# Kernel tuning notes

Hardware: AMD Instinct MI355X
Metric: run time of the kernel (lower is better)

## Reference

```python
import jax, jax.numpy as jnp
import numpy as np

D = 512; NH = 8; FF = 2048; LE = 6; LD = 6; V = 97; SM = 512; SQ = 128; B = 16
EPS = 1e-5


def _posenc(length, depth):
    half = depth // 2
    pos = jnp.arange(length, dtype=jnp.float32)[:, None]
    dep = jnp.arange(half, dtype=jnp.float32)[None, :] / half
    ang = pos / (10000.0 ** dep)
    return jnp.concatenate([jnp.sin(ang), jnp.cos(ang)], axis=-1)  # [length, depth]


def _ln(x, w, b):
    mu = jnp.mean(x, axis=-1, keepdims=True)
    var = jnp.mean((x - mu) ** 2, axis=-1, keepdims=True)
    return (x - mu) * jax.lax.rsqrt(var + EPS) * w + b


def _heads(t, S, Bt):
    return t.reshape(S, Bt * NH, D // NH).transpose(1, 0, 2)  # [B*H, S, dk]


def _self_attn(x, wqkv, bqkv, wo, bo, causal):
    S, Bt, _ = x.shape
    qkv = x @ wqkv.T + bqkv
    q, k, v = jnp.split(qkv, 3, axis=-1)
    q = _heads(q, S, Bt); k = _heads(k, S, Bt); v = _heads(v, S, Bt)
    scores = jnp.einsum('hqd,hkd->hqk', q, k) / jnp.sqrt(jnp.asarray(D // NH, x.dtype))
    if causal:
        mask = jnp.triu(jnp.ones((S, S), bool), 1)
        scores = jnp.where(mask[None], -jnp.inf, scores)
    attn = jax.nn.softmax(scores, axis=-1)
    out = jnp.einsum('hqk,hkd->hqd', attn, v).transpose(1, 0, 2).reshape(S, Bt, D)
    return out @ wo.T + bo


def _cross_attn(query, memory, wq, bq, wk, bk, wv, bv, wo, bo):
    Sq, Bt, _ = query.shape
    Sm = memory.shape[0]
    q = _heads(query @ wq.T + bq, Sq, Bt)
    k = _heads(memory @ wk.T + bk, Sm, Bt)
    v = _heads(memory @ wv.T + bv, Sm, Bt)
    scores = jnp.einsum('hqd,hkd->hqk', q, k) / jnp.sqrt(jnp.asarray(D // NH, query.dtype))
    attn = jax.nn.softmax(scores, axis=-1)
    out = jnp.einsum('hqk,hkd->hqd', attn, v).transpose(1, 0, 2).reshape(Sq, Bt, D)
    return out @ wo.T + bo


def _forward(src, tokens, tok_emb,
             enc_qkv_w, enc_qkv_b, enc_out_w, enc_out_b,
             enc_l1_w, enc_l1_b, enc_l2_w, enc_l2_b,
             enc_n1_w, enc_n1_b, enc_n2_w, enc_n2_b,
             dec_qkv_w, dec_qkv_b, dec_sout_w, dec_sout_b,
             dec_q_w, dec_q_b, dec_k_w, dec_k_b, dec_v_w, dec_v_b,
             dec_cout_w, dec_cout_b,
             dec_l1_w, dec_l1_b, dec_l2_w, dec_l2_b,
             dec_n1_w, dec_n1_b, dec_n2_w, dec_n2_b, dec_n3_w, dec_n3_b,
             out_w, out_b):
    # ---- encoder ----
    x = src  # [SM, B, D]
    for i in range(LE):
        x2 = _self_attn(x, enc_qkv_w[i], enc_qkv_b[i], enc_out_w[i], enc_out_b[i], causal=False)
        x = _ln(x + x2, enc_n1_w[i], enc_n1_b[i])
        x2 = jax.nn.relu(x @ enc_l1_w[i].T + enc_l1_b[i]) @ enc_l2_w[i].T + enc_l2_b[i]
        x = _ln(x + x2, enc_n2_w[i], enc_n2_b[i])
    memory = x
    # ---- decoder ----
    tgt = tok_emb[tokens] + _posenc(tokens.shape[0], D)[:, None, :]  # [SQ, B, D]
    for i in range(LD):
        x2 = _self_attn(tgt, dec_qkv_w[i], dec_qkv_b[i], dec_sout_w[i], dec_sout_b[i], causal=True)
        tgt = _ln(tgt + x2, dec_n1_w[i], dec_n1_b[i])
        x2 = _cross_attn(tgt, memory, dec_q_w[i], dec_q_b[i], dec_k_w[i], dec_k_b[i],
                         dec_v_w[i], dec_v_b[i], dec_cout_w[i], dec_cout_b[i])
        tgt = _ln(tgt + x2, dec_n2_w[i], dec_n2_b[i])
        x2 = jax.nn.relu(tgt @ dec_l1_w[i].T + dec_l1_b[i]) @ dec_l2_w[i].T + dec_l2_b[i]
        tgt = _ln(tgt + x2, dec_n3_w[i], dec_n3_b[i])
    return tgt @ out_w.T + out_b  # [SQ, B, V]


def setup_inputs() -> dict:
    key = jax.random.key(0)
    ks = iter(jax.random.split(key, 64))
    g = lambda shape: jax.random.normal(next(ks), shape, dtype=jnp.float32) * 0.02
    inp = {
        'src': jax.random.normal(next(ks), (SM, B, D), dtype=jnp.float32),
        'tokens': jax.random.randint(next(ks), (SQ, B), 0, V),
        'tok_emb': g((V, D)),
        'enc_qkv_w': g((LE, 3 * D, D)), 'enc_qkv_b': g((LE, 3 * D)),
        'enc_out_w': g((LE, D, D)), 'enc_out_b': g((LE, D)),
        'enc_l1_w': g((LE, FF, D)), 'enc_l1_b': g((LE, FF)),
        'enc_l2_w': g((LE, D, FF)), 'enc_l2_b': g((LE, D)),
        'enc_n1_w': jnp.ones((LE, D)), 'enc_n1_b': jnp.zeros((LE, D)),
        'enc_n2_w': jnp.ones((LE, D)), 'enc_n2_b': jnp.zeros((LE, D)),
        'dec_qkv_w': g((LD, 3 * D, D)), 'dec_qkv_b': g((LD, 3 * D)),
        'dec_sout_w': g((LD, D, D)), 'dec_sout_b': g((LD, D)),
        'dec_q_w': g((LD, D, D)), 'dec_q_b': g((LD, D)),
        'dec_k_w': g((LD, D, D)), 'dec_k_b': g((LD, D)),
        'dec_v_w': g((LD, D, D)), 'dec_v_b': g((LD, D)),
        'dec_cout_w': g((LD, D, D)), 'dec_cout_b': g((LD, D)),
        'dec_l1_w': g((LD, FF, D)), 'dec_l1_b': g((LD, FF)),
        'dec_l2_w': g((LD, D, FF)), 'dec_l2_b': g((LD, D)),
        'dec_n1_w': jnp.ones((LD, D)), 'dec_n1_b': jnp.zeros((LD, D)),
        'dec_n2_w': jnp.ones((LD, D)), 'dec_n2_b': jnp.zeros((LD, D)),
        'dec_n3_w': jnp.ones((LD, D)), 'dec_n3_b': jnp.zeros((LD, D)),
        'out_w': g((V, D)), 'out_b': g((V,)),
    }
    return inp


def reference(src, tokens, tok_emb,
              enc_qkv_w, enc_qkv_b, enc_out_w, enc_out_b,
              enc_l1_w, enc_l1_b, enc_l2_w, enc_l2_b,
              enc_n1_w, enc_n1_b, enc_n2_w, enc_n2_b,
              dec_qkv_w, dec_qkv_b, dec_sout_w, dec_sout_b,
              dec_q_w, dec_q_b, dec_k_w, dec_k_b, dec_v_w, dec_v_b,
              dec_cout_w, dec_cout_b,
              dec_l1_w, dec_l1_b, dec_l2_w, dec_l2_b,
              dec_n1_w, dec_n1_b, dec_n2_w, dec_n2_b, dec_n3_w, dec_n3_b,
              out_w, out_b):
    return _forward(src, tokens, tok_emb,
                    enc_qkv_w, enc_qkv_b, enc_out_w, enc_out_b,
                    enc_l1_w, enc_l1_b, enc_l2_w, enc_l2_b,
                    enc_n1_w, enc_n1_b, enc_n2_w, enc_n2_b,
                    dec_qkv_w, dec_qkv_b, dec_sout_w, dec_sout_b,
                    dec_q_w, dec_q_b, dec_k_w, dec_k_b, dec_v_w, dec_v_b,
                    dec_cout_w, dec_cout_b,
                    dec_l1_w, dec_l1_b, dec_l2_w, dec_l2_b,
                    dec_n1_w, dec_n1_b, dec_n2_w, dec_n2_b, dec_n3_w, dec_n3_b,
                    out_w, out_b)
```

## Files before the change

kernel.cpp:

```cpp
#include <hip/hip_runtime.h>
#include <hip/hip_bf16.h>
#include <cstddef>
#include <cstdint>

#define D_MODEL 512
#define BATCH 16
#define EPS_LN 1e-5f

typedef __bf16 bf16x8 __attribute__((ext_vector_type(8)));
typedef float f32x4 __attribute__((ext_vector_type(4)));
typedef unsigned short u16x8 __attribute__((ext_vector_type(8)));
typedef unsigned short u16x4 __attribute__((ext_vector_type(4)));
typedef unsigned short u16x2 __attribute__((ext_vector_type(2)));

__device__ __forceinline__ void gload_lds16(const void* g, void* l) {
    __builtin_amdgcn_global_load_lds(
        (const __attribute__((address_space(1))) void*)g,
        (__attribute__((address_space(3))) void*)l,
        16, 0, 0);
}

template <int BM, int OUTBF16, int SWAP>
__global__ __launch_bounds__(512) void gemm_mfma(
    const __bf16* __restrict__ A, const __bf16* __restrict__ W,
    const __bf16* __restrict__ W2, int wsplit,
    const float* __restrict__ bias, const float* __restrict__ bias2, int bsplit,
    void* __restrict__ Cout, __bf16* __restrict__ VTout, int m_vt0, int log2S,
    int N, int Mlim, int MS, int K, int relu, int permrow)
{
    constexpr int MR     = BM / 32;
    constexpr int WRSPAN = BM / 2;
    constexpr int ABYTES = BM * 128;
    constexpr int PA     = ABYTES / 8192;
    constexpr int BUFB   = ABYTES + 16384;

    __shared__ __align__(16) char smem[2 * BUFB];

    const int tid  = threadIdx.x;
    const int lane = tid & 63;
    const int wid  = tid >> 6;
    const int wrow = wid >> 2;
    const int wcol = wid & 3;
    const int row0 = blockIdx.y * BM;
    const int col0 = blockIdx.x * 128;

    const int lrow  = lane & 15;
    const int lhalf = lane >> 4;
    const int koff0 = ((lhalf) ^ (lrow & 7)) * 16;
    const int koff1 = ((4 + lhalf) ^ (lrow & 7)) * 16;

    const int srow = tid >> 3;
    const int slot = tid & 7;
    const int sg   = slot ^ (srow & 7);

    f32x4 acc[MR][2] = {};

    const __bf16* Wsel = W;
    int wc0 = col0;
    if (col0 >= wsplit) { Wsel = W2; wc0 = col0 - wsplit; }

    const __bf16* Abase = A + (size_t)(row0 + srow) * K + sg * 8;
    const __bf16* Wbase = Wsel + (size_t)(wc0 + srow) * K + sg * 8;

    auto stage = [&](char* buf, int kt) {
#pragma unroll
        for (int p = 0; p < PA; ++p)
            gload_lds16(Abase + (size_t)p * 64 * K + kt, buf + p * 8192 + tid * 16);
#pragma unroll
        for (int p = 0; p < 2; ++p)
            gload_lds16(Wbase + (size_t)p * 64 * K + kt,
                        buf + ABYTES + p * 8192 + tid * 16);
    };

    stage(smem, 0);
    const int nkt = K >> 6;
    int cur = 0;
    for (int kt = 0; kt < nkt; ++kt) {
        __syncthreads();
        if (kt + 1 < nkt) stage(smem + (cur ^ 1) * BUFB, (kt + 1) * 64);
        const char* aB = smem + cur * BUFB + (wrow * WRSPAN + lrow) * 128;
        const char* wB = smem + cur * BUFB + ABYTES + (wcol * 32 + lrow) * 128;
#pragma unroll
        for (int ks = 0; ks < 2; ++ks) {
            const int ko = ks ? koff1 : koff0;
            bf16x8 af[MR], bfr[2];
#pragma unroll
            for (int m = 0; m < MR; ++m) af[m]  = *(const bf16x8*)(aB + m * 2048 + ko);
#pragma unroll
            for (int n = 0; n < 2; ++n)  bfr[n] = *(const bf16x8*)(wB + n * 2048 + ko);
            if (SWAP) {
#pragma unroll
                for (int m = 0; m < MR; ++m)
#pragma unroll
                    for (int n = 0; n < 2; ++n)
                        acc[m][n] = __builtin_amdgcn_mfma_f32_16x16x32_bf16(
                            bfr[n], af[m], acc[m][n], 0, 0, 0);
            } else {
#pragma unroll
                for (int m = 0; m < MR; ++m)
#pragma unroll
                    for (int n = 0; n < 2; ++n)
                        acc[m][n] = __builtin_amdgcn_mfma_f32_16x16x32_bf16(
                            af[m], bfr[n], acc[m][n], 0, 0, 0);
            }
        }
        cur ^= 1;
    }

    if (SWAP) {
#pragma unroll
        for (int m = 0; m < MR; ++m) {
            const int r = row0 + wrow * WRSPAN + m * 16 + lrow;
#pragma unroll
            for (int n = 0; n < 2; ++n) {
                const int c0 = col0 + wcol * 32 + n * 16 + lhalf * 4;
                const float4 bv = *(const float4*)(bias + c0);
                float o0 = acc[m][n][0] + bv.x, o1 = acc[m][n][1] + bv.y;
                float o2 = acc[m][n][2] + bv.z, o3 = acc[m][n][3] + bv.w;
                if (relu) {
                    o0 = fmaxf(o0, 0.f); o1 = fmaxf(o1, 0.f);
                    o2 = fmaxf(o2, 0.f); o3 = fmaxf(o3, 0.f);
                }
                if (OUTBF16) {
                    union { __bf16 h4[4]; u16x4 u; } pk;
                    pk.h4[0] = (__bf16)o0; pk.h4[1] = (__bf16)o1;
                    pk.h4[2] = (__bf16)o2; pk.h4[3] = (__bf16)o3;
                    *(u16x4*)((__bf16*)Cout + (size_t)r * MS + c0) = pk.u;
                } else {
                    *(float4*)((float*)Cout + (size_t)r * MS + c0) =
                        make_float4(o0, o1, o2, o3);
                }
            }
        }
    } else {
        const int orow = row0 + wrow * WRSPAN + lhalf * 4;
        const int ocol = col0 + wcol * 32 + lrow;
        const int smask = (1 << log2S) - 1;
#pragma unroll
        for (int n = 0; n < 2; ++n) {
            const int c = ocol + n * 16;
            if (c >= m_vt0) {
                const int cv = c - m_vt0;
                const int hh = cv >> 6, dd = cv & 63;
                const float bv = (bias2 && c >= bsplit) ? bias2[c - bsplit] : bias[c];
#pragma unroll
                for (int m = 0; m < MR; ++m) {
                    const int rr = orow + m * 16;
                    const int bb = rr >> log2S, ss = rr & smask;
                    union { __bf16 h4[4]; u16x4 u; } pk;
#pragma unroll
                    for (int j = 0; j < 4; ++j)
                        pk.h4[j] = (__bf16)(acc[m][n][j] + bv);
                    *(u16x4*)(VTout + (((size_t)((bb * 8 + hh) * 64 + dd)) << log2S) + ss) = pk.u;
                }
            } else if (c < Mlim) {
                const float bv = (bias2 && c >= bsplit) ? bias2[c - bsplit] : bias[c];
#pragma unroll
                for (int m = 0; m < MR; ++m) {
#pragma unroll
                    for (int j = 0; j < 4; ++j) {
                        int rr = orow + m * 16 + j;
                        if (permrow) rr = ((rr & smask) * BATCH) + (rr >> log2S);
                        float v = acc[m][n][j] + bv;
                        if (relu) v = fmaxf(v, 0.f);
                        if (OUTBF16) ((__bf16*)Cout)[(size_t)rr * MS + c] = (__bf16)v;
                        else         ((float*)Cout)[(size_t)rr * MS + c] = v;
                    }
                }
            }
        }
    }
}

template <int CAUSAL>
__global__ __launch_bounds__(256) void attn_mfma(
    const __bf16* __restrict__ Qb, const __bf16* __restrict__ Kb,
    const __bf16* __restrict__ VT, __bf16* __restrict__ Op,
    int Sq, int Skv, int qstride, int kstride, int koff, float scale)
{
    __shared__ __align__(16) char smem[40960];
    const int tid = threadIdx.x;
    const int l   = tid & 63;
    const int w   = tid >> 6;
    char* Psm = smem + 32768 + w * 2048;

    const int qc = blockIdx.x;
    const int h  = blockIdx.y;
    const int b  = blockIdx.z;
    const int l15 = l & 15;
    const int g   = l >> 4;
    const int sw  = l15 & 7;

    const int sq = qc * 64 + w * 16 + l15;
    const __bf16* qrow = Qb + ((size_t)(b * Sq + sq)) * qstride + h * 64 + g * 8;
    const bf16x8 qf0 = *(const bf16x8*)(qrow);
    const bf16x8 qf1 = *(const bf16x8*)(qrow + 32);

    const int srow = tid >> 3;
    const int slot = tid & 7;

    auto stageKV = [&](char* buf, int kc) {
#pragma unroll
        for (int p = 0; p < 2; ++p) {
            const int r   = p * 32 + srow;
            const int sgo = (slot ^ (r & 7)) * 8;
            const __bf16* ksrc = Kb + ((size_t)(b * Skv + kc * 64 + r)) * kstride
                                    + koff + h * 64 + sgo;
            gload_lds16(ksrc, buf + (p * 256 + tid) * 16);
            const __bf16* vsrc = VT + ((size_t)((b * 8 + h) * 64 + r)) * Skv
                                    + kc * 64 + sgo;
            gload_lds16(vsrc, buf + 8192 + (p * 256 + tid) * 16);
        }
    };

    f32x4 acc[4] = {};
    float m_run = -1e30f, l_run = 0.f;

    const int nkc = CAUSAL ? (qc + 1) : (Skv >> 6);
    stageKV(smem, 0);
    int cur = 0;
    for (int kc = 0; kc < nkc; ++kc) {
        __syncthreads();
        if (kc + 1 < nkc) stageKV(smem + (cur ^ 1) * 16384, kc + 1);
        const char* Ksm = smem + cur * 16384;
        const char* Vsm = Ksm + 8192;

        f32x4 st[4];
#pragma unroll
        for (int f = 0; f < 4; ++f) {
            const char* kr = Ksm + (f * 16 + l15) * 128;
            bf16x8 ka0 = *(const bf16x8*)(kr + ((g ^ sw) * 16));
            bf16x8 ka1 = *(const bf16x8*)(kr + (((4 + g) ^ sw) * 16));
            f32x4 z = {};
            z = __builtin_amdgcn_mfma_f32_16x16x32_bf16(ka0, qf0, z, 0, 0, 0);
            st[f] = __builtin_amdgcn_mfma_f32_16x16x32_bf16(ka1, qf1, z, 0, 0, 0);
        }

        float rmax = -1e30f;
#pragma unroll
        for (int f = 0; f < 4; ++f)
#pragma unroll
            for (int j = 0; j < 4; ++j) {
                float v = st[f][j] * scale;
                if (CAUSAL) {
                    if (kc * 64 + f * 16 + g * 4 + j > sq) v = -1e30f;
                }
                st[f][j] = v;
                rmax = fmaxf(rmax, v);
            }
        rmax = fmaxf(rmax, __shfl_xor(rmax, 16, 64));
        rmax = fmaxf(rmax, __shfl_xor(rmax, 32, 64));
        const float mn = fmaxf(m_run, rmax);
        const float corr = __expf(m_run - mn);
        m_run = mn;
        float rsum = 0.f;
#pragma unroll
        for (int f = 0; f < 4; ++f)
#pragma unroll
            for (int j = 0; j < 4; ++j) {
                float p = __expf(st[f][j] - mn);
                st[f][j] = p;
                rsum += p;
            }
        rsum += __shfl_xor(rsum, 16, 64);
        rsum += __shfl_xor(rsum, 32, 64);
        l_run = l_run * corr + rsum;

#pragma unroll
        for (int j = 0; j < 4; ++j) {
            const float cj = __shfl(corr, g * 20 + j, 64);
            acc[0][j] *= cj; acc[1][j] *= cj; acc[2][j] *= cj; acc[3][j] *= cj;
        }

#pragma unroll
        for (int f = 0; f < 4; ++f)
#pragma unroll
            for (int j2 = 0; j2 < 2; ++j2) {
                union { __bf16 h2[2]; unsigned u; } cv;
                cv.h2[0] = (__bf16)st[f][2 * j2];
                cv.h2[1] = (__bf16)st[f][2 * j2 + 1];
                const int key0 = 16 * f + 4 * g + 2 * j2;
                const int byte = l15 * 128 + (((key0 >> 3) ^ sw) * 16) + (key0 & 7) * 2;
                *(unsigned*)(Psm + byte) = cv.u;
            }

#pragma unroll
        for (int ks = 0; ks < 2; ++ks) {
            const int so = ((4 * ks + g) ^ sw) * 16;
            bf16x8 pa = *(const bf16x8*)(Psm + l15 * 128 + so);
#pragma unroll
            for (int n = 0; n < 4; ++n) {
                bf16x8 vb = *(const bf16x8*)(Vsm + (n * 16 + l15) * 128 + so);
                acc[n] = __builtin_amdgcn_mfma_f32_16x16x32_bf16(pa, vb, acc[n], 0, 0, 0);
            }
        }
        cur ^= 1;
    }

    const float inv = 1.f / l_run;
#pragma unroll
    for (int j = 0; j < 4; ++j) {
        const float ij = __shfl(inv, g * 20 + j, 64);
        const int s = qc * 64 + w * 16 + g * 4 + j;
        __bf16* orow = Op + ((size_t)(b * Sq + s)) * D_MODEL + h * 64 + l15;
#pragma unroll
        for (int n = 0; n < 4; ++n)
            orow[n * 16] = (__bf16)(acc[n][j] * ij);
    }
}

__global__ __launch_bounds__(256) void add_ln(
    const float* __restrict__ X, const __bf16* __restrict__ Y,
    const float* __restrict__ w, const float* __restrict__ bias,
    float* __restrict__ Of, __bf16* __restrict__ Oh)
{
    const int t   = blockIdx.x;
    const int tid = threadIdx.x;
    const float2 x2 = *(const float2*)(X + (size_t)t * D_MODEL + tid * 2);
    const u16x2 yv = *(const u16x2*)(Y + (size_t)t * D_MODEL + tid * 2);
    union { u16x2 u; __bf16 h2[2]; } yc; yc.u = yv;
    float v0 = x2.x + (float)yc.h2[0], v1 = x2.y + (float)yc.h2[1];
    float sum = v0 + v1;
    float sq  = v0 * v0 + v1 * v1;
#pragma unroll
    for (int off = 32; off; off >>= 1) {
        sum += __shfl_xor(sum, off);
        sq  += __shfl_xor(sq, off);
    }
    __shared__ float ssum[4], ssq[4];
    const int wid = tid >> 6;
    if ((tid & 63) == 0) { ssum[wid] = sum; ssq[wid] = sq; }
    __syncthreads();
    sum = ssum[0] + ssum[1] + ssum[2] + ssum[3];
    sq  = ssq[0] + ssq[1] + ssq[2] + ssq[3];

    const float mu  = sum * (1.f / D_MODEL);
    const float var = sq * (1.f / D_MODEL) - mu * mu;
    const float rs  = rsqrtf(var + EPS_LN);
    const float2 w2 = *(const float2*)(w + tid * 2);
    const float2 b2 = *(const float2*)(bias + tid * 2);
    float o0 = (v0 - mu) * rs * w2.x + b2.x;
    float o1 = (v1 - mu) * rs * w2.y + b2.y;
    *(float2*)(Of + (size_t)t * D_MODEL + tid * 2) = make_float2(o0, o1);
    union { __bf16 h2[2]; u16x2 u; } cv;
    cv.h2[0] = (__bf16)o0; cv.h2[1] = (__bf16)o1;
    *(u16x2*)(Oh + (size_t)t * D_MODEL + tid * 2) = cv.u;
}

__global__ __launch_bounds__(256) void permute_src(
    const float* __restrict__ src, float* __restrict__ Of, __bf16* __restrict__ Oh)
{
    const int t = blockIdx.x;
    const int b = t >> 9, s = t & 511;
    const int tid = threadIdx.x;
    const float2 v = *(const float2*)(src + ((size_t)(s * BATCH + b)) * D_MODEL + tid * 2);
    *(float2*)(Of + (size_t)t * D_MODEL + tid * 2) = v;
    union { __bf16 h2[2]; u16x2 u; } cv;
    cv.h2[0] = (__bf16)v.x; cv.h2[1] = (__bf16)v.y;
    *(u16x2*)(Oh + (size_t)t * D_MODEL + tid * 2) = cv.u;
}

__global__ __launch_bounds__(256) void embed_pos(
    const int* __restrict__ tokens, const float* __restrict__ emb,
    float* __restrict__ Of, __bf16* __restrict__ Oh)
{
    const int t   = blockIdx.x;
    const int b   = t >> 7, s = t & 127;
    const int tid = threadIdx.x;
    const int tok = tokens[s * BATCH + b];
    const float C = 9.210340371976184f / 256.f;
    const int d = tid * 2;
    const int j = (d < 256) ? d : (d - 256);
    float a0 = (float)s * expf(-(float)j * C);
    float a1 = (float)s * expf(-(float)(j + 1) * C);
    float pe0 = (d < 256) ? sinf(a0) : cosf(a0);
    float pe1 = (d < 256) ? sinf(a1) : cosf(a1);
    const float2 e2 = *(const float2*)(emb + (size_t)tok * D_MODEL + d);
    float o0 = e2.x + pe0, o1 = e2.y + pe1;
    *(float2*)(Of + (size_t)t * D_MODEL + d) = make_float2(o0, o1);
    union { __bf16 h2[2]; u16x2 u; } cv;
    cv.h2[0] = (__bf16)o0; cv.h2[1] = (__bf16)o1;
    *(u16x2*)(Oh + (size_t)t * D_MODEL + d) = cv.u;
}

struct CvtSeg { const float* s; __bf16* d; int n8; };
struct CvtArgs { CvtSeg seg[12]; int tot8; };

__global__ __launch_bounds__(256) void cvt_multi(CvtArgs a)
{
    const int stride = gridDim.x * 256;
    int sgi = 0;
    int base = 0;
    for (int u = blockIdx.x * 256 + threadIdx.x; u < a.tot8; u += stride) {
        while (u - base >= a.seg[sgi].n8) { base += a.seg[sgi].n8; ++sgi; }
        const int v = u - base;
        const float4 f0 = ((const float4*)a.seg[sgi].s)[v * 2];
        const float4 f1 = ((const float4*)a.seg[sgi].s)[v * 2 + 1];
        union { __bf16 h[8]; u16x8 u; } c;
        c.h[0] = (__bf16)f0.x; c.h[1] = (__bf16)f0.y;
        c.h[2] = (__bf16)f0.z; c.h[3] = (__bf16)f0.w;
        c.h[4] = (__bf16)f1.x; c.h[5] = (__bf16)f1.y;
        c.h[6] = (__bf16)f1.z; c.h[7] = (__bf16)f1.w;
        ((u16x8*)a.seg[sgi].d)[v] = c.u;
    }
}

__global__ __launch_bounds__(256) void pad_outw(
    const float* __restrict__ w, __bf16* __restrict__ o)
{
    const int idx = blockIdx.x * 256 + threadIdx.x;
    const int r = idx >> 9;
    const int c = idx & 511;
    o[idx] = (__bf16)(r < 97 ? w[r * 512 + c] : 0.f);
}

extern "C" void kernel_launch(void* const* d_in, const int* in_sizes, int n_in,
                              void* d_out, int out_size, void* d_ws, size_t ws_size,
                              hipStream_t stream)
{
    const float* src     = (const float*)d_in[0];
    const int*   tokens  = (const int*)d_in[1];
    const float* tok_emb = (const float*)d_in[2];
    const float* enc_qkv_w = (const float*)d_in[3];
    const float* enc_qkv_b = (const float*)d_in[4];
    const float* enc_out_w = (const float*)d_in[5];
    const float* enc_out_b = (const float*)d_in[6];
    const float* enc_l1_w  = (const float*)d_in[7];
    const float* enc_l1_b  = (const float*)d_in[8];
    const float* enc_l2_w  = (const float*)d_in[9];
    const float* enc_l2_b  = (const float*)d_in[10];
    const float* enc_n1_w  = (const float*)d_in[11];
    const float* enc_n1_b  = (const float*)d_in[12];
    const float* enc_n2_w  = (const float*)d_in[13];
    const float* enc_n2_b  = (const float*)d_in[14];
    const float* dec_qkv_w = (const float*)d_in[15];
    const float* dec_qkv_b = (const float*)d_in[16];
    const float* dec_sout_w = (const float*)d_in[17];
    const float* dec_sout_b = (const float*)d_in[18];
    const float* dec_q_w   = (const float*)d_in[19];
    const float* dec_q_b   = (const float*)d_in[20];
    const float* dec_k_w   = (const float*)d_in[21];
    const float* dec_k_b   = (const float*)d_in[22];
    const float* dec_v_w   = (const float*)d_in[23];
    const float* dec_v_b   = (const float*)d_in[24];
    const float* dec_cout_w = (const float*)d_in[25];
    const float* dec_cout_b = (const float*)d_in[26];
    const float* dec_l1_w  = (const float*)d_in[27];
    const float* dec_l1_b  = (const float*)d_in[28];
    const float* dec_l2_w  = (const float*)d_in[29];
    const float* dec_l2_b  = (const float*)d_in[30];
    const float* dec_n1_w  = (const float*)d_in[31];
    const float* dec_n1_b  = (const float*)d_in[32];
    const float* dec_n2_w  = (const float*)d_in[33];
    const float* dec_n2_b  = (const float*)d_in[34];
    const float* dec_n3_w  = (const float*)d_in[35];
    const float* dec_n3_b  = (const float*)d_in[36];
    const float* out_w     = (const float*)d_in[37];
    const float* out_b     = (const float*)d_in[38];

    const int NE = 512 * BATCH;
    const int ND = 128 * BATCH;
    const float scale = 0.125f;
    const int BIG = 1 << 30;

    char* w8 = (char*)d_ws;
    float*  Ax_f = (float*) (w8 + 0);
    float*  T_f  = (float*) (w8 + 16777216);
    __bf16* Ax_h = (__bf16*)(w8 + 20971520);
    __bf16* T_h  = (__bf16*)(w8 + 29360128);
    __bf16* AO_h = (__bf16*)(w8 + 31457280);
    __bf16* Y_h  = (__bf16*)(w8 + 39845888);
    __bf16* VT   = (__bf16*)(w8 + 48234496);
    __bf16* OWp  = (__bf16*)(w8 + 56623104);
    char*   Gb   = w8 + 56754176;
    __bf16* Gqk  = (__bf16*)Gb;
    __bf16* Gh   = (__bf16*)Gb;
    __bf16* Gq   = (__bf16*)Gb;
    __bf16* Gk   = (__bf16*)(Gb + 2097152);
    __bf16* WB   = (__bf16*)(w8 + 90308608);

    const bool upfront = ws_size >= (size_t)178388992;

    auto gemmS = [&](const __bf16* Am, const __bf16* Wm, const float* bv,
                     void* C, int N, int M, int K, int relu) {
        const int nb128 = (M / 128) * (N / 128);
        if (nb128 >= 512) {
            dim3 grid(M / 128, N / 128);
            gemm_mfma<128, 1, 1><<<grid, 512, 0, stream>>>(
                Am, Wm, nullptr, BIG, bv, nullptr, 0, C, nullptr, BIG, 0,
                N, M, M, K, relu, 0);
        } else {
            dim3 grid(M / 128, N / 64);
            gemm_mfma<64, 1, 1><<<grid, 512, 0, stream>>>(
                Am, Wm, nullptr, BIG, bv, nullptr, 0, C, nullptr, BIG, 0,
                N, M, M, K, relu, 0);
        }
    };
    auto gemmN = [&](const __bf16* Am, const __bf16* Wm, const __bf16* W2m, int wsplit,
                     const float* bv, const float* bv2, int bsplit,
                     void* C, __bf16* VTp, int m_vt0, int log2S,
                     int N, int M, int MS, int K, bool outbf, int permrow) {
        const int nb128 = ((M + 127) / 128) * (N / 128);
        if (nb128 >= 512) {
            dim3 grid((M + 127) / 128, N / 128);
            if (outbf) gemm_mfma<128, 1, 0><<<grid, 512, 0, stream>>>(
                Am, Wm, W2m, wsplit, bv, bv2, bsplit, C, VTp, m_vt0, log2S,
                N, M, MS, K, 0, permrow);
            else       gemm_mfma<128, 0, 0><<<grid, 512, 0, stream>>>(
                Am, Wm, W2m, wsplit, bv, bv2, bsplit, C, VTp, m_vt0, log2S,
                N, M, MS, K, 0, permrow);
        } else {
            dim3 grid((M + 127) / 128, N / 64);
            if (outbf) gemm_mfma<64, 1, 0><<<grid, 512, 0, stream>>>(
                Am, Wm, W2m, wsplit, bv, bv2, bsplit, C, VTp, m_vt0, log2S,
                N, M, MS, K, 0, permrow);
            else       gemm_mfma<64, 0, 0><<<grid, 512, 0, stream>>>(
                Am, Wm, W2m, wsplit, bv, bv2, bsplit, C, VTp, m_vt0, log2S,
                N, M, MS, K, 0, permrow);
        }
    };
    auto cvt = [&](CvtArgs& a, int blocks) {
        int tot = 0;
        for (int i = 0; i < 12; ++i) tot += a.seg[i].n8;
        a.tot8 = tot;
        cvt_multi<<<blocks, 256, 0, stream>>>(a);
    };

    permute_src<<<NE, 256, 0, stream>>>(src, Ax_f, Ax_h);
    pad_outw<<<256, 256, 0, stream>>>(out_w, OWp);

    __bf16* WencQKV = WB;
    __bf16* WencOUT = WencQKV + 4718592;
    __bf16* WencL1  = WencOUT + 1572864;
    __bf16* WencL2  = WencL1 + 6291456;
    __bf16* WdecQKV = WencL2 + 6291456;
    __bf16* WdecSOUT = WdecQKV + 4718592;
    __bf16* WdecQ   = WdecSOUT + 1572864;
    __bf16* WdecK   = WdecQ + 1572864;
    __bf16* WdecV   = WdecK + 1572864;
    __bf16* WdecCOUT = WdecV + 1572864;
    __bf16* WdecL1  = WdecCOUT + 1572864;
    __bf16* WdecL2  = WdecL1 + 6291456;

    if (upfront) {
        CvtArgs a = {};
        a.seg[0]  = { enc_qkv_w,  WencQKV,  4718592 / 8 };
        a.seg[1]  = { enc_out_w,  WencOUT,  1572864 / 8 };
        a.seg[2]  = { enc_l1_w,   WencL1,   6291456 / 8 };
        a.seg[3]  = { enc_l2_w,   WencL2,   6291456 / 8 };
        a.seg[4]  = { dec_qkv_w,  WdecQKV,  4718592 / 8 };
        a.seg[5]  = { dec_sout_w, WdecSOUT, 1572864 / 8 };
        a.seg[6]  = { dec_q_w,    WdecQ,    1572864 / 8 };
        a.seg[7]  = { dec_k_w,    WdecK,    1572864 / 8 };
        a.seg[8]  = { dec_v_w,    WdecV,    1572864 / 8 };
        a.seg[9]  = { dec_cout_w, WdecCOUT, 1572864 / 8 };
        a.seg[10] = { dec_l1_w,   WdecL1,   6291456 / 8 };
        a.seg[11] = { dec_l2_w,   WdecL2,   6291456 / 8 };
        cvt(a, 4096);
    }

    for (int i = 0; i < 6; ++i) {
        __bf16 *wqkv, *wout, *wl1, *wl2;
        if (upfront) {
            wqkv = WencQKV + (size_t)i * 786432;
            wout = WencOUT + (size_t)i * 262144;
            wl1  = WencL1 + (size_t)i * 1048576;
            wl2  = WencL2 + (size_t)i * 1048576;
        } else {
            wqkv = WB; wout = WB + 786432; wl1 = WB + 1048576; wl2 = WB + 2097152;
            CvtArgs a = {};
            a.seg[0] = { enc_qkv_w + (size_t)i * 786432,  wqkv, 786432 / 8 };
            a.seg[1] = { enc_out_w + (size_t)i * 262144,  wout, 262144 / 8 };
            a.seg[2] = { enc_l1_w  + (size_t)i * 1048576, wl1, 1048576 / 8 };
            a.seg[3] = { enc_l2_w  + (size_t)i * 1048576, wl2, 1048576 / 8 };
            cvt(a, 1024);
        }

        gemmN(Ax_h, wqkv, nullptr, BIG, enc_qkv_b + (size_t)i * 1536, nullptr, 0,
              Gqk, VT, 1024, 9, NE, 1536, 1024, 512, true, 0);
        attn_mfma<0><<<dim3(8, 8, BATCH), 256, 0, stream>>>(
            Gqk, Gqk, VT, AO_h, 512, 512, 1024, 1024, 512, scale);
        gemmS(AO_h, wout, enc_out_b + (size_t)i * 512, Y_h, NE, 512, 512, 0);
        add_ln<<<NE, 256, 0, stream>>>(Ax_f, Y_h,
                                       enc_n1_w + (size_t)i * 512, enc_n1_b + (size_t)i * 512,
                                       Ax_f, Ax_h);
        gemmS(Ax_h, wl1, enc_l1_b + (size_t)i * 2048, Gh, NE, 2048, 512, 1);
        gemmS(Gh, wl2, enc_l2_b + (size_t)i * 512, Y_h, NE, 512, 2048, 0);
        add_ln<<<NE, 256, 0, stream>>>(Ax_f, Y_h,
                                       enc_n2_w + (size_t)i * 512, enc_n2_b + (size_t)i * 512,
                                       Ax_f, Ax_h);
    }

    embed_pos<<<ND, 256, 0, stream>>>(tokens, tok_emb, T_f, T_h);
    for (int i = 0; i < 6; ++i) {
        __bf16 *dqkv, *dsout, *dq, *dk, *dv, *dcout, *dl1, *dl2;
        if (upfront) {
            dqkv  = WdecQKV + (size_t)i * 786432;
            dsout = WdecSOUT + (size_t)i * 262144;
            dq    = WdecQ + (size_t)i * 262144;
            dk    = WdecK + (size_t)i * 262144;
            dv    = WdecV + (size_t)i * 262144;
            dcout = WdecCOUT + (size_t)i * 262144;
            dl1   = WdecL1 + (size_t)i * 1048576;
            dl2   = WdecL2 + (size_t)i * 1048576;
        } else {
            dqkv = WB; dsout = WB + 786432; dq = WB + 1048576; dk = WB + 1310720;
            dv = WB + 1572864; dcout = WB + 1835008; dl1 = WB + 2097152; dl2 = WB + 3145728;
            CvtArgs a = {};
            a.seg[0] = { dec_qkv_w  + (size_t)i * 786432,  dqkv,  786432 / 8 };
            a.seg[1] = { dec_sout_w + (size_t)i * 262144,  dsout, 262144 / 8 };
            a.seg[2] = { dec_q_w    + (size_t)i * 262144,  dq,    262144 / 8 };
            a.seg[3] = { dec_k_w    + (size_t)i * 262144,  dk,    262144 / 8 };
            a.seg[4] = { dec_v_w    + (size_t)i * 262144,  dv,    262144 / 8 };
            a.seg[5] = { dec_cout_w + (size_t)i * 262144,  dcout, 262144 / 8 };
            a.seg[6] = { dec_l1_w   + (size_t)i * 1048576, dl1,  1048576 / 8 };
            a.seg[7] = { dec_l2_w   + (size_t)i * 1048576, dl2,  1048576 / 8 };
            cvt(a, 1024);
        }

        gemmN(T_h, dqkv, nullptr, BIG, dec_qkv_b + (size_t)i * 1536, nullptr, 0,
              Gqk, VT, 1024, 7, ND, 1536, 1024, 512, true, 0);
        attn_mfma<1><<<dim3(2, 8, BATCH), 256, 0, stream>>>(
            Gqk, Gqk, VT, AO_h, 128, 128, 1024, 1024, 512, scale);
        gemmS(AO_h, dsout, dec_sout_b + (size_t)i * 512, Y_h, ND, 512, 512, 0);
        add_ln<<<ND, 256, 0, stream>>>(T_f, Y_h,
                                       dec_n1_w + (size_t)i * 512, dec_n1_b + (size_t)i * 512,
                                       T_f, T_h);
        gemmS(T_h, dq, dec_q_b + (size_t)i * 512, Gq, ND, 512, 512, 0);
        gemmN(Ax_h, dk, dv, 512, dec_k_b + (size_t)i * 512, dec_v_b + (size_t)i * 512, 512,
              Gk, VT, 512, 9, NE, 1024, 512, 512, true, 0);
        attn_mfma<0><<<dim3(2, 8, BATCH), 256, 0, stream>>>(
            Gq, Gk, VT, AO_h, 128, 512, 512, 512, 0, scale);
        gemmS(AO_h, dcout, dec_cout_b + (size_t)i * 512, Y_h, ND, 512, 512, 0);
        add_ln<<<ND, 256, 0, stream>>>(T_f, Y_h,
                                       dec_n2_w + (size_t)i * 512, dec_n2_b + (size_t)i * 512,
                                       T_f, T_h);
        gemmS(T_h, dl1, dec_l1_b + (size_t)i * 2048, Gh, ND, 2048, 512, 1);
        gemmS(Gh, dl2, dec_l2_b + (size_t)i * 512, Y_h, ND, 512, 2048, 0);
        add_ln<<<ND, 256, 0, stream>>>(T_f, Y_h,
                                       dec_n3_w + (size_t)i * 512, dec_n3_b + (size_t)i * 512,
                                       T_f, T_h);
    }

    gemmN(T_h, OWp, nullptr, BIG, out_b, nullptr, 0,
          (float*)d_out, nullptr, BIG, 7, ND, 97, 97, 512, false, 1);
}
```

Before: 1.534 ms.

## Fuse output-projection GEMMs with residual add and LayerNorm; add XCD-aware block swizzle

```diff
diff --git a/kernel.cpp b/kernel.cpp
--- a/kernel.cpp
+++ b/kernel.cpp
@@ -18,6 +18,12 @@
         (const __attribute__((address_space(1))) void*)g,
         (__attribute__((address_space(3))) void*)l,
         16, 0, 0);
+}
+
+__device__ __forceinline__ int xcd_swz(int wg, int nwg) {
+    const int q = nwg >> 3, r = nwg & 7;
+    const int x = wg & 7, p = wg >> 3;
+    return (x < r ? x * (q + 1) : r * (q + 1) + (x - r) * q) + p;
 }
 
 template <int BM, int OUTBF16, int SWAP>
@@ -26,7 +32,7 @@
     const __bf16* __restrict__ W2, int wsplit,
     const float* __restrict__ bias, const float* __restrict__ bias2, int bsplit,
     void* __restrict__ Cout, __bf16* __restrict__ VTout, int m_vt0, int log2S,
-    int N, int Mlim, int MS, int K, int relu, int permrow)
+    int gx, int Mlim, int MS, int K, int relu, int permrow)
 {
     constexpr int MR     = BM / 32;
     constexpr int WRSPAN = BM / 2;
@@ -41,8 +47,10 @@
     const int wid  = tid >> 6;
     const int wrow = wid >> 2;
     const int wcol = wid & 3;
-    const int row0 = blockIdx.y * BM;
-    const int col0 = blockIdx.x * 128;
+
+    const int wgid = xcd_swz(blockIdx.x, gridDim.x);
+    const int row0 = (wgid / gx) * BM;
+    const int col0 = (wgid % gx) * 128;
 
     const int lrow  = lane & 15;
     const int lhalf = lane >> 4;
@@ -172,6 +180,143 @@
     }
 }
 
+__global__ __launch_bounds__(512) void gemm_ln(
+    const __bf16* __restrict__ A, const __bf16* __restrict__ W,
+    const float* __restrict__ bias, const float* __restrict__ Xres,
+    const float* __restrict__ lnw, const float* __restrict__ lnb,
+    float* __restrict__ Of, __bf16* __restrict__ Oh, int K)
+{
+    constexpr int WB2  = 512 * 128;
+    constexpr int AB2  = 32 * 128;
+    constexpr int BUFB = WB2 + AB2;
+    __shared__ __align__(16) char smem[2 * BUFB + 2176];
+    float* redS = (float*)(smem + 2 * BUFB);
+    float* redQ = (float*)(smem + 2 * BUFB + 1024);
+
+    const int tid   = threadIdx.x;
+    const int lane  = tid & 63;
+    const int w     = tid >> 6;
+    const int lrow  = lane & 15;
+    const int lhalf = lane >> 4;
+    const int row0  = blockIdx.x * 32;
+
+    const int srow = tid >> 3;
+    const int slot = tid & 7;
+    const int sg   = slot ^ (srow & 7);
+
+    const int koff0 = ((lhalf) ^ (lrow & 7)) * 16;
+    const int koff1 = ((4 + lhalf) ^ (lrow & 7)) * 16;
+
+    f32x4 acc[2][4] = {};
+
+    auto stage = [&](char* buf, int kt) {
+#pragma unroll
+        for (int p = 0; p < 8; ++p) {
+            const int wr = p * 64 + srow;
+            gload_lds16(W + (size_t)wr * K + kt + sg * 8, buf + p * 8192 + tid * 16);
+        }
+        if (tid < 256) {
+            gload_lds16(A + (size_t)(row0 + srow) * K + kt + sg * 8,
+                        buf + WB2 + tid * 16);
+        }
+    };
+
+    stage(smem, 0);
+    const int nkt = K >> 6;
+    int cur = 0;
+    for (int kt = 0; kt < nkt; ++kt) {
+        __syncthreads();
+        if (kt + 1 < nkt) stage(smem + (cur ^ 1) * BUFB, (kt + 1) * 64);
+        const char* wB = smem + cur * BUFB;
+        const char* aB = wB + WB2;
+#pragma unroll
+        for (int ks = 0; ks < 2; ++ks) {
+            const int ko = ks ? koff1 : koff0;
+            bf16x8 af[2], bfr[4];
+#pragma unroll
+            for (int m = 0; m < 2; ++m)
+                af[m] = *(const bf16x8*)(aB + (m * 16 + lrow) * 128 + ko);
+#pragma unroll
+            for (int n = 0; n < 4; ++n)
+                bfr[n] = *(const bf16x8*)(wB + (w * 64 + n * 16 + lrow) * 128 + ko);
+#pragma unroll
+            for (int m = 0; m < 2; ++m)
+#pragma unroll
+                for (int n = 0; n < 4; ++n)
+                    acc[m][n] = __builtin_amdgcn_mfma_f32_16x16x32_bf16(
+                        bfr[n], af[m], acc[m][n], 0, 0, 0);
+        }
+        cur ^= 1;
+    }
+
+    float vals[2][4][4];
+    float s[2] = {0.f, 0.f}, q[2] = {0.f, 0.f};
+#pragma unroll
+    for (int m = 0; m < 2; ++m) {
+        const int r = row0 + m * 16 + lrow;
+#pragma unroll
+        for (int n = 0; n < 4; ++n) {
+            const int c0 = w * 64 + n * 16 + lhalf * 4;
+            const float4 bv = *(const float4*)(bias + c0);
+            const float4 xv = *(const float4*)(Xres + (size_t)r * 512 + c0);
+            const float v0 = (float)(__bf16)(acc[m][n][0] + bv.x) + xv.x;
+            const float v1 = (float)(__bf16)(acc[m][n][1] + bv.y) + xv.y;
+            const float v2 = (float)(__bf16)(acc[m][n][2] + bv.z) + xv.z;
+            const float v3 = (float)(__bf16)(acc[m][n][3] + bv.w) + xv.w;
+            vals[m][n][0] = v0; vals[m][n][1] = v1;
+            vals[m][n][2] = v2; vals[m][n][3] = v3;
+            s[m] += v0 + v1 + v2 + v3;
+            q[m] += v0 * v0 + v1 * v1 + v2 * v2 + v3 * v3;
+        }
+    }
+#pragma unroll
+    for (int m = 0; m < 2; ++m) {
+        s[m] += __shfl_xor(s[m], 16, 64); s[m] += __shfl_xor(s[m], 32, 64);
+        q[m] += __shfl_xor(q[m], 16, 64); q[m] += __shfl_xor(q[m], 32, 64);
+    }
+    __syncthreads();
+    if (lhalf == 0) {
+#pragma unroll
+        for (int m = 0; m < 2; ++m) {
+            redS[(m * 16 + lrow) * 8 + w] = s[m];
+            redQ[(m * 16 + lrow) * 8 + w] = q[m];
+        }
+    }
+    __syncthreads();
+    float mu[2], rstd[2];
+#pragma unroll
+    for (int m = 0; m < 2; ++m) {
+        const int rr = m * 16 + lrow;
+        float ts = 0.f, tq = 0.f;
+#pragma unroll
+        for (int ww = 0; ww < 8; ++ww) {
+            ts += redS[rr * 8 + ww];
+            tq += redQ[rr * 8 + ww];
+        }
+        mu[m] = ts * (1.f / 512.f);
+        rstd[m] = rsqrtf(tq * (1.f / 512.f) - mu[m] * mu[m] + EPS_LN);
+    }
+#pragma unroll
+    for (int m = 0; m < 2; ++m) {
+        const int r = row0 + m * 16 + lrow;
+#pragma unroll
+        for (int n = 0; n < 4; ++n) {
+            const int c0 = w * 64 + n * 16 + lhalf * 4;
+            const float4 wv = *(const float4*)(lnw + c0);
+            const float4 bb = *(const float4*)(lnb + c0);
+            const float o0 = (vals[m][n][0] - mu[m]) * rstd[m] * wv.x + bb.x;
+            const float o1 = (vals[m][n][1] - mu[m]) * rstd[m] * wv.y + bb.y;
+            const float o2 = (vals[m][n][2] - mu[m]) * rstd[m] * wv.z + bb.z;
+            const float o3 = (vals[m][n][3] - mu[m]) * rstd[m] * wv.w + bb.w;
+            *(float4*)(Of + (size_t)r * 512 + c0) = make_float4(o0, o1, o2, o3);
+            union { __bf16 h4[4]; u16x4 u; } pk;
+            pk.h4[0] = (__bf16)o0; pk.h4[1] = (__bf16)o1;
+            pk.h4[2] = (__bf16)o2; pk.h4[3] = (__bf16)o3;
+            *(u16x4*)(Oh + (size_t)r * 512 + c0) = pk.u;
+        }
+    }
+}
+
 template <int CAUSAL>
 __global__ __launch_bounds__(256) void attn_mfma(
     const __bf16* __restrict__ Qb, const __bf16* __restrict__ Kb,
@@ -307,44 +452,6 @@
         for (int n = 0; n < 4; ++n)
             orow[n * 16] = (__bf16)(acc[n][j] * ij);
     }
-}
-
-__global__ __launch_bounds__(256) void add_ln(
-    const float* __restrict__ X, const __bf16* __restrict__ Y,
-    const float* __restrict__ w, const float* __restrict__ bias,
-    float* __restrict__ Of, __bf16* __restrict__ Oh)
-{
-    const int t   = blockIdx.x;
-    const int tid = threadIdx.x;
-    const float2 x2 = *(const float2*)(X + (size_t)t * D_MODEL + tid * 2);
-    const u16x2 yv = *(const u16x2*)(Y + (size_t)t * D_MODEL + tid * 2);
-    union { u16x2 u; __bf16 h2[2]; } yc; yc.u = yv;
-    float v0 = x2.x + (float)yc.h2[0], v1 = x2.y + (float)yc.h2[1];
-    float sum = v0 + v1;
-    float sq  = v0 * v0 + v1 * v1;
-#pragma unroll
-    for (int off = 32; off; off >>= 1) {
-        sum += __shfl_xor(sum, off);
-        sq  += __shfl_xor(sq, off);
-    }
-    __shared__ float ssum[4], ssq[4];
-    const int wid = tid >> 6;
-    if ((tid & 63) == 0) { ssum[wid] = sum; ssq[wid] = sq; }
-    __syncthreads();
-    sum = ssum[0] + ssum[1] + ssum[2] + ssum[3];
-    sq  = ssq[0] + ssq[1] + ssq[2] + ssq[3];
-
-    const float mu  = sum * (1.f / D_MODEL);
-    const float var = sq * (1.f / D_MODEL) - mu * mu;
-    const float rs  = rsqrtf(var + EPS_LN);
-    const float2 w2 = *(const float2*)(w + tid * 2);
-    const float2 b2 = *(const float2*)(bias + tid * 2);
-    float o0 = (v0 - mu) * rs * w2.x + b2.x;
-    float o1 = (v1 - mu) * rs * w2.y + b2.y;
-    *(float2*)(Of + (size_t)t * D_MODEL + tid * 2) = make_float2(o0, o1);
-    union { __bf16 h2[2]; u16x2 u; } cv;
-    cv.h2[0] = (__bf16)o0; cv.h2[1] = (__bf16)o1;
-    *(u16x2*)(Oh + (size_t)t * D_MODEL + tid * 2) = cv.u;
 }
 
 __global__ __launch_bounds__(256) void permute_src(
@@ -469,7 +576,6 @@
     __bf16* Ax_h = (__bf16*)(w8 + 20971520);
     __bf16* T_h  = (__bf16*)(w8 + 29360128);
     __bf16* AO_h = (__bf16*)(w8 + 31457280);
-    __bf16* Y_h  = (__bf16*)(w8 + 39845888);
     __bf16* VT   = (__bf16*)(w8 + 48234496);
     __bf16* OWp  = (__bf16*)(w8 + 56623104);
     char*   Gb   = w8 + 56754176;
@@ -484,40 +590,43 @@
     auto gemmS = [&](const __bf16* Am, const __bf16* Wm, const float* bv,
                      void* C, int N, int M, int K, int relu) {
         const int nb128 = (M / 128) * (N / 128);
+        const int gx = M / 128;
         if (nb128 >= 512) {
-            dim3 grid(M / 128, N / 128);
-            gemm_mfma<128, 1, 1><<<grid, 512, 0, stream>>>(
+            gemm_mfma<128, 1, 1><<<gx * (N / 128), 512, 0, stream>>>(
                 Am, Wm, nullptr, BIG, bv, nullptr, 0, C, nullptr, BIG, 0,
-                N, M, M, K, relu, 0);
+                gx, M, M, K, relu, 0);
         } else {
-            dim3 grid(M / 128, N / 64);
-            gemm_mfma<64, 1, 1><<<grid, 512, 0, stream>>>(
+            gemm_mfma<64, 1, 1><<<gx * (N / 64), 512, 0, stream>>>(
                 Am, Wm, nullptr, BIG, bv, nullptr, 0, C, nullptr, BIG, 0,
-                N, M, M, K, relu, 0);
+                gx, M, M, K, relu, 0);
         }
     };
     auto gemmN = [&](const __bf16* Am, const __bf16* Wm, const __bf16* W2m, int wsplit,
                      const float* bv, const float* bv2, int bsplit,
                      void* C, __bf16* VTp, int m_vt0, int log2S,
                      int N, int M, int MS, int K, bool outbf, int permrow) {
-        const int nb128 = ((M + 127) / 128) * (N / 128);
+        const int gx = (M + 127) / 128;
+        const int nb128 = gx * (N / 128);
         if (nb128 >= 512) {
-            dim3 grid((M + 127) / 128, N / 128);
-            if (outbf) gemm_mfma<128, 1, 0><<<grid, 512, 0, stream>>>(
+            if (outbf) gemm_mfma<128, 1, 0><<<gx * (N / 128), 512, 0, stream>>>(
                 Am, Wm, W2m, wsplit, bv, bv2, bsplit, C, VTp, m_vt0, log2S,
-                N, M, MS, K, 0, permrow);
-            else       gemm_mfma<128, 0, 0><<<grid, 512, 0, stream>>>(
+                gx, M, MS, K, 0, permrow);
+            else       gemm_mfma<128, 0, 0><<<gx * (N / 128), 512, 0, stream>>>(
                 Am, Wm, W2m, wsplit, bv, bv2, bsplit, C, VTp, m_vt0, log2S,
-                N, M, MS, K, 0, permrow);
+                gx, M, MS, K, 0, permrow);
         } else {
-            dim3 grid((M + 127) / 128, N / 64);
-            if (outbf) gemm_mfma<64, 1, 0><<<grid, 512, 0, stream>>>(
+            if (outbf) gemm_mfma<64, 1, 0><<<gx * (N / 64), 512, 0, stream>>>(
                 Am, Wm, W2m, wsplit, bv, bv2, bsplit, C, VTp, m_vt0, log2S,
-                N, M, MS, K, 0, permrow);
-            else       gemm_mfma<64, 0, 0><<<grid, 512, 0, stream>>>(
+                gx, M, MS, K, 0, permrow);
+            else       gemm_mfma<64, 0, 0><<<gx * (N / 64), 512, 0, stream>>>(
                 Am, Wm, W2m, wsplit, bv, bv2, bsplit, C, VTp, m_vt0, log2S,
-                N, M, MS, K, 0, permrow);
-        }
+                gx, M, MS, K, 0, permrow);
+        }
+    };
+    auto gemmLN = [&](const __bf16* Am, const __bf16* Wm, const float* bv,
+                      const float* Xr, const float* lw, const float* lb,
+                      float* Of, __bf16* Oh, int N, int K) {
+        gemm_ln<<<N / 32, 512, 0, stream>>>(Am, Wm, bv, Xr, lw, lb, Of, Oh, K);
     };
     auto cvt = [&](CvtArgs& a, int blocks) {
         int tot = 0;
@@ -580,15 +689,13 @@
               Gqk, VT, 1024, 9, NE, 1536, 1024, 512, true, 0);
         attn_mfma<0><<<dim3(8, 8, BATCH), 256, 0, stream>>>(
             Gqk, Gqk, VT, AO_h, 512, 512, 1024, 1024, 512, scale);
-        gemmS(AO_h, wout, enc_out_b + (size_t)i * 512, Y_h, NE, 512, 512, 0);
-        add_ln<<<NE, 256, 0, stream>>>(Ax_f, Y_h,
-                                       enc_n1_w + (size_t)i * 512, enc_n1_b + (size_t)i * 512,
-                                       Ax_f, Ax_h);
+        gemmLN(AO_h, wout, enc_out_b + (size_t)i * 512, Ax_f,
+               enc_n1_w + (size_t)i * 512, enc_n1_b + (size_t)i * 512,
+               Ax_f, Ax_h, NE, 512);
         gemmS(Ax_h, wl1, enc_l1_b + (size_t)i * 2048, Gh, NE, 2048, 512, 1);
-        gemmS(Gh, wl2, enc_l2_b + (size_t)i * 512, Y_h, NE, 512, 2048, 0);
-        add_ln<<<NE, 256, 0, stream>>>(Ax_f, Y_h,
-                                       enc_n2_w + (size_t)i * 512, enc_n2_b + (size_t)i * 512,
-                                       Ax_f, Ax_h);
+        gemmLN(Gh, wl2, enc_l2_b + (size_t)i * 512, Ax_f,
+               enc_n2_w + (size_t)i * 512, enc_n2_b + (size_t)i * 512,
+               Ax_f, Ax_h, NE, 2048);
     }
 
     embed_pos<<<ND, 256, 0, stream>>>(tokens, tok_emb, T_f, T_h);
@@ -622,24 +729,21 @@
               Gqk, VT, 1024, 7, ND, 1536, 1024, 512, true, 0);
         attn_mfma<1><<<dim3(2, 8, BATCH), 256, 0, stream>>>(
             Gqk, Gqk, VT, AO_h, 128, 128, 1024, 1024, 512, scale);
-        gemmS(AO_h, dsout, dec_sout_b + (size_t)i * 512, Y_h, ND, 512, 512, 0);
-        add_ln<<<ND, 256, 0, stream>>>(T_f, Y_h,
-                                       dec_n1_w + (size_t)i * 512, dec_n1_b + (size_t)i * 512,
-                                       T_f, T_h);
+        gemmLN(AO_h, dsout, dec_sout_b + (size_t)i * 512, T_f,
+               dec_n1_w + (size_t)i * 512, dec_n1_b + (size_t)i * 512,
+               T_f, T_h, ND, 512);
         gemmS(T_h, dq, dec_q_b + (size_t)i * 512, Gq, ND, 512, 512, 0);
         gemmN(Ax_h, dk, dv, 512, dec_k_b + (size_t)i * 512, dec_v_b + (size_t)i * 512, 512,
               Gk, VT, 512, 9, NE, 1024, 512, 512, true, 0);
         attn_mfma<0><<<dim3(2, 8, BATCH), 256, 0, stream>>>(
             Gq, Gk, VT, AO_h, 128, 512, 512, 512, 0, scale);
-        gemmS(AO_h, dcout, dec_cout_b + (size_t)i * 512, Y_h, ND, 512, 512, 0);
-        add_ln<<<ND, 256, 0, stream>>>(T_f, Y_h,
-                                       dec_n2_w + (size_t)i * 512, dec_n2_b + (size_t)i * 512,
-                                       T_f, T_h);
+        gemmLN(AO_h, dcout, dec_cout_b + (size_t)i * 512, T_f,
+               dec_n2_w + (size_t)i * 512, dec_n2_b + (size_t)i * 512,
+               T_f, T_h, ND, 512);
         gemmS(T_h, dl1, dec_l1_b + (size_t)i * 2048, Gh, ND, 2048, 512, 1);
-        gemmS(Gh, dl2, dec_l2_b + (size_t)i * 512, Y_h, ND, 512, 2048, 0);
-        add_ln<<<ND, 256, 0, stream>>>(T_f, Y_h,
-                                       dec_n3_w + (size_t)i * 512, dec_n3_b + (size_t)i * 512,
-                                       T_f, T_h);
+        gemmLN(Gh, dl2, dec_l2_b + (size_t)i * 512, T_f,
+               dec_n3_w + (size_t)i * 512, dec_n3_b + (size_t)i * 512,
+               T_f, T_h, ND, 2048);
     }
 
     gemmN(T_h, OWp, nullptr, BIG, out_b, nullptr, 0,
```

Result: slower. 1.695 ms (+10.5%).
